# Optimization experiments

Hardware: AMD Instinct MI355X
Metric: run time of the kernel (lower is better)

Reference implementation:

```python
import jax, jax.numpy as jnp
import numpy as np

N_AUTHORS = 50000
N_PAPERS = 100000
N_NODES = N_AUTHORS + N_PAPERS
N_EDGES = 1200000
EMB_DIM = 64
NUM_LAYERS = 3


def setup_inputs() -> dict:
    key = jax.random.key(0)
    k1, k2, k3, k4, k5 = jax.random.split(key, 5)
    author_embedding = jax.random.normal(k1, (N_AUTHORS, EMB_DIM), dtype=jnp.float32)
    paper_embedding = jax.random.normal(k2, (N_PAPERS, EMB_DIM), dtype=jnp.float32)
    adj_rows = jax.random.randint(k3, (N_EDGES,), 0, N_NODES, dtype=jnp.int32)
    adj_cols = jax.random.randint(k4, (N_EDGES,), 0, N_NODES, dtype=jnp.int32)
    # symmetric-normalized adjacency values are small positive floats
    adj_vals = jax.random.uniform(k5, (N_EDGES,), dtype=jnp.float32) * 0.1
    return {
        "author_embedding": author_embedding,
        "paper_embedding": paper_embedding,
        "adj_rows": adj_rows,
        "adj_cols": adj_cols,
        "adj_vals": adj_vals,
    }


def _spmm(adj_rows, adj_cols, adj_vals, x):
    # sparse [N,N] @ dense [N,d] via gather + segment_sum
    msgs = adj_vals[:, None] * x[adj_cols]  # [E, d]
    return jax.ops.segment_sum(msgs, adj_rows, num_segments=N_NODES)


def reference(author_embedding, paper_embedding, adj_rows, adj_cols, adj_vals):
    ego = jnp.concatenate([author_embedding, paper_embedding], axis=0)  # [N, d]
    acc = ego
    x = ego
    for _ in range(NUM_LAYERS):
        x = _spmm(adj_rows, adj_cols, adj_vals, x)
        acc = acc + x
    out = acc / jnp.float32(NUM_LAYERS + 1)  # mean over layer outputs
    out_author = out[:N_AUTHORS]
    out_paper = out[N_AUTHORS:]
    return ego, out_author, out_paper
```

## Files before the change

### kernel.cpp

```cpp
#include <hip/hip_runtime.h>

#define N_AUTHORS 50000
#define N_PAPERS  100000
#define N_NODES   150000
#define N_EDGES   1200000
#define EMB       64

#define BSHIFT 10
#define K_B    ((N_NODES + 1023) >> 10)
#define CHUNK  4096
#define NBLK_A ((N_EDGES + CHUNK - 1) / CHUNK)
#define NSC    (K_B * NBLK_A)
#define NBS1   ((NSC + 1023) / 1024)

typedef float v2f __attribute__((ext_vector_type(2)));

__device__ __forceinline__ ushort f2bf(float f) {
    unsigned u = __float_as_uint(f);
    return (ushort)((u + 0x7fffu + ((u >> 16) & 1u)) >> 16);
}
#define bfLO(u) __uint_as_float((u) << 16)
#define bfHI(u) __uint_as_float((u) & 0xffff0000u)

__global__ void lgcn_hist_init(const int* __restrict__ rows,
                               unsigned* __restrict__ counts,
                               const float* __restrict__ a,
                               const float* __restrict__ p,
                               float* __restrict__ ego_out,
                               ushort* __restrict__ x0) {
    __shared__ unsigned h[K_B];
    int t = threadIdx.x;
    if (blockIdx.x < NBLK_A) {
        for (int i = t; i < K_B; i += blockDim.x) h[i] = 0;
        __syncthreads();
        int base = blockIdx.x * CHUNK;
        int end  = base + CHUNK; if (end > N_EDGES) end = N_EDGES;
        for (int e = base + t; e < end; e += blockDim.x)
            atomicAdd(&h[rows[e] >> BSHIFT], 1u);
        __syncthreads();
        for (int i = t; i < K_B; i += blockDim.x)
            counts[(size_t)i * NBLK_A + blockIdx.x] = h[i];
    } else {
        size_t i = (size_t)(blockIdx.x - NBLK_A) * blockDim.x + t;
        const size_t n4  = (size_t)N_NODES  * EMB / 4;
        const size_t au4 = (size_t)N_AUTHORS * EMB / 4;
        if (i >= n4) return;
        float4 v = (i < au4) ? ((const float4*)a)[i] : ((const float4*)p)[i - au4];
        ((float4*)ego_out)[i] = v;
        ushort4 b;
        b.x = f2bf(v.x); b.y = f2bf(v.y); b.z = f2bf(v.z); b.w = f2bf(v.w);
        ((ushort4*)x0)[i] = b;
    }
}

__global__ void lgcn_scan_l1(const unsigned* __restrict__ counts,
                             unsigned* __restrict__ scanned,
                             unsigned* __restrict__ btot) {
    __shared__ unsigned s[1024];
    int t = threadIdx.x;
    int i = blockIdx.x * 1024 + t;
    unsigned v = (i < NSC) ? counts[i] : 0u;
    s[t] = v;
    __syncthreads();
    for (int d = 1; d < 1024; d <<= 1) {
        unsigned u = (t >= d) ? s[t - d] : 0u;
        __syncthreads();
        s[t] += u;
        __syncthreads();
    }
    if (i < NSC) scanned[i] = s[t] - v;
    if (t == 1023) btot[blockIdx.x] = s[1023];
}

__global__ void lgcn_scan_l2(const unsigned* __restrict__ btot,
                             unsigned* __restrict__ btot_ex) {
    __shared__ unsigned s[64];
    int t = threadIdx.x;
    unsigned v = (t < NBS1) ? btot[t] : 0u;
    s[t] = v;
    __syncthreads();
    for (int d = 1; d < 64; d <<= 1) {
        unsigned u = (t >= d) ? s[t - d] : 0u;
        __syncthreads();
        s[t] += u;
        __syncthreads();
    }
    btot_ex[t] = s[t] - v;
}

__device__ __forceinline__ unsigned scan_at(const unsigned* scanned,
                                            const unsigned* btot_ex, unsigned idx) {
    return scanned[idx] + btot_ex[idx >> 10];
}

__global__ void lgcn_a1_bin(const int* __restrict__ rows,
                            const int* __restrict__ cols,
                            const float* __restrict__ vals,
                            const unsigned* __restrict__ scanned,
                            const unsigned* __restrict__ btot_ex,
                            float2* __restrict__ stage) {
    __shared__ unsigned cur[K_B];
    int t = threadIdx.x;
    for (int i = t; i < K_B; i += blockDim.x)
        cur[i] = scan_at(scanned, btot_ex, (unsigned)i * NBLK_A + blockIdx.x);
    __syncthreads();
    int base = blockIdx.x * CHUNK;
    int end  = base + CHUNK; if (end > N_EDGES) end = N_EDGES;
    for (int e = base + t; e < end; e += blockDim.x) {
        int r = rows[e];
        unsigned pos = atomicAdd(&cur[r >> BSHIFT], 1u);
        unsigned packed = ((unsigned)(r & 1023) << 18) | (unsigned)cols[e];
        stage[pos] = make_float2(__uint_as_float(packed), vals[e]);
    }
}

__global__ void lgcn_place(const unsigned* __restrict__ scanned,
                           const unsigned* __restrict__ btot_ex,
                           const float2* __restrict__ stage,
                           float2* __restrict__ se,
                           unsigned* __restrict__ row_start) {
    __shared__ unsigned cur[1 << BSHIFT];
    __shared__ unsigned tsum[256];
    int b  = blockIdx.x;
    int rb = b << BSHIFT;
    int nrows = N_NODES - rb; if (nrows > (1 << BSHIFT)) nrows = 1 << BSHIFT;
    int t = threadIdx.x;

    unsigned base  = scan_at(scanned, btot_ex, (unsigned)b * NBLK_A);
    unsigned span1 = (b + 1 < K_B)
                   ? scan_at(scanned, btot_ex, (unsigned)(b + 1) * NBLK_A)
                   : N_EDGES;

    for (int i = t; i < (1 << BSHIFT); i += 256) cur[i] = 0;
    __syncthreads();
    for (unsigned p = base + t; p < span1; p += 256)
        atomicAdd(&cur[__float_as_uint(stage[p].x) >> 18], 1u);
    __syncthreads();

    unsigned c[4], s = 0;
#pragma unroll
    for (int k = 0; k < 4; ++k) { c[k] = cur[t * 4 + k]; s += c[k]; }
    tsum[t] = s;
    __syncthreads();
    for (int d = 1; d < 256; d <<= 1) {
        unsigned u = (t >= d) ? tsum[t - d] : 0u;
        __syncthreads();
        tsum[t] += u;
        __syncthreads();
    }
    unsigned run = base + (tsum[t] - s);
    __syncthreads();
#pragma unroll
    for (int k = 0; k < 4; ++k) {
        int i = t * 4 + k;
        cur[i] = run;
        if (i < nrows) row_start[rb + i] = run;
        run += c[k];
    }
    if (b == K_B - 1 && t == 0) row_start[N_NODES] = N_EDGES;
    __syncthreads();

    for (unsigned p = base + t; p < span1; p += 256) {
        float2 v = stage[p];
        unsigned u = __float_as_uint(v.x);
        unsigned pos = atomicAdd(&cur[u >> 18], 1u);
        se[pos] = make_float2(__int_as_float((int)(u & 0x3FFFFu)), v.y);
    }
}

template <int MODE>
__global__ void lgcn_spmm(const unsigned* __restrict__ rs,
                          const float2* __restrict__ se,
                          const ushort* __restrict__ xb,
                          const unsigned char* __restrict__ x8,
                          ushort* __restrict__ y16,
                          unsigned char* __restrict__ y8,
                          const ushort* __restrict__ egob,
                          const ushort* __restrict__ y1b,
                          float* __restrict__ out) {
    int w    = blockIdx.x * (blockDim.x >> 6) + (threadIdx.x >> 6);
    int lane = threadIdx.x & 63;
    int r0   = w << 1;
    if (r0 >= N_NODES) return;
    unsigned jA   = rs[r0];
    unsigned endA = rs[r0 + 1];
    unsigned jB   = endA;
    unsigned endB = rs[r0 + 2];
    const int g  = lane >> 3;
    const int d8 = (lane & 7) << 3;
    float a0=0.f,a1=0.f,a2=0.f,a3=0.f,a4=0.f,a5=0.f,a6=0.f,a7=0.f;
    float b0=0.f,b1=0.f,b2=0.f,b3=0.f,b4=0.f,b5=0.f,b6=0.f,b7=0.f;

#define BATCH8(JB, END, P)                                                    \
    {                                                                         \
        unsigned idx = (JB) + g;                                              \
        float2 e;                                                             \
        if (idx < (END)) e = se[idx];                                         \
        else { e.x = __int_as_float(0); e.y = 0.f; }                          \
        if constexpr (MODE == 0) {                                            \
            const uint4 xv = *(const uint4*)(xb + ((size_t)__float_as_int(e.x) << 6) + d8); \
            P##0 += e.y * bfLO(xv.x); P##1 += e.y * bfHI(xv.x);               \
            P##2 += e.y * bfLO(xv.y); P##3 += e.y * bfHI(xv.y);               \
            P##4 += e.y * bfLO(xv.z); P##5 += e.y * bfHI(xv.z);               \
            P##6 += e.y * bfLO(xv.w); P##7 += e.y * bfHI(xv.w);               \
        } else {                                                              \
            const uint2 xv = *(const uint2*)(x8 + ((size_t)__float_as_int(e.x) << 6) + d8); \
            v2f p01 = __builtin_amdgcn_cvt_pk_f32_fp8((int)xv.x, false);      \
            v2f p23 = __builtin_amdgcn_cvt_pk_f32_fp8((int)xv.x, true);       \
            v2f p45 = __builtin_amdgcn_cvt_pk_f32_fp8((int)xv.y, false);      \
            v2f p67 = __builtin_amdgcn_cvt_pk_f32_fp8((int)xv.y, true);       \
            P##0 += e.y * p01.x; P##1 += e.y * p01.y;                         \
            P##2 += e.y * p23.x; P##3 += e.y * p23.y;                         \
            P##4 += e.y * p45.x; P##5 += e.y * p45.y;                         \
            P##6 += e.y * p67.x; P##7 += e.y * p67.y;                         \
        }                                                                     \
    }

    BATCH8(jA, endA, a)
    BATCH8(jB, endB, b)
    jA += 8; jB += 8;
    while (jA < endA) { BATCH8(jA, endA, a) jA += 8; }
    while (jB < endB) { BATCH8(jB, endB, b) jB += 8; }
#undef BATCH8

    a0 += __shfl_xor(a0, 8, 64); a0 += __shfl_xor(a0, 16, 64); a0 += __shfl_xor(a0, 32, 64);
    a1 += __shfl_xor(a1, 8, 64); a1 += __shfl_xor(a1, 16, 64); a1 += __shfl_xor(a1, 32, 64);
    a2 += __shfl_xor(a2, 8, 64); a2 += __shfl_xor(a2, 16, 64); a2 += __shfl_xor(a2, 32, 64);
    a3 += __shfl_xor(a3, 8, 64); a3 += __shfl_xor(a3, 16, 64); a3 += __shfl_xor(a3, 32, 64);
    a4 += __shfl_xor(a4, 8, 64); a4 += __shfl_xor(a4, 16, 64); a4 += __shfl_xor(a4, 32, 64);
    a5 += __shfl_xor(a5, 8, 64); a5 += __shfl_xor(a5, 16, 64); a5 += __shfl_xor(a5, 32, 64);
    a6 += __shfl_xor(a6, 8, 64); a6 += __shfl_xor(a6, 16, 64); a6 += __shfl_xor(a6, 32, 64);
    a7 += __shfl_xor(a7, 8, 64); a7 += __shfl_xor(a7, 16, 64); a7 += __shfl_xor(a7, 32, 64);
    b0 += __shfl_xor(b0, 8, 64); b0 += __shfl_xor(b0, 16, 64); b0 += __shfl_xor(b0, 32, 64);
    b1 += __shfl_xor(b1, 8, 64); b1 += __shfl_xor(b1, 16, 64); b1 += __shfl_xor(b1, 32, 64);
    b2 += __shfl_xor(b2, 8, 64); b2 += __shfl_xor(b2, 16, 64); b2 += __shfl_xor(b2, 32, 64);
    b3 += __shfl_xor(b3, 8, 64); b3 += __shfl_xor(b3, 16, 64); b3 += __shfl_xor(b3, 32, 64);
    b4 += __shfl_xor(b4, 8, 64); b4 += __shfl_xor(b4, 16, 64); b4 += __shfl_xor(b4, 32, 64);
    b5 += __shfl_xor(b5, 8, 64); b5 += __shfl_xor(b5, 16, 64); b5 += __shfl_xor(b5, 32, 64);
    b6 += __shfl_xor(b6, 8, 64); b6 += __shfl_xor(b6, 16, 64); b6 += __shfl_xor(b6, 32, 64);
    b7 += __shfl_xor(b7, 8, 64); b7 += __shfl_xor(b7, 16, 64); b7 += __shfl_xor(b7, 32, 64);

    if (g == 0) {
#define EMIT(ROW, P)                                                          \
    {                                                                         \
        size_t o = ((size_t)(ROW) << 6) + d8;                                 \
        if constexpr (MODE == 2) {                                            \
            uint4 ue = *(const uint4*)(egob + o);                             \
            uint4 u1 = *(const uint4*)(y1b + o);                              \
            uint2 u2 = *(const uint2*)(x8 + o);                               \
            v2f q01 = __builtin_amdgcn_cvt_pk_f32_fp8((int)u2.x, false);      \
            v2f q23 = __builtin_amdgcn_cvt_pk_f32_fp8((int)u2.x, true);       \
            v2f q45 = __builtin_amdgcn_cvt_pk_f32_fp8((int)u2.y, false);      \
            v2f q67 = __builtin_amdgcn_cvt_pk_f32_fp8((int)u2.y, true);       \
            float4 lo, hi;                                                    \
            lo.x = 0.25f * (bfLO(ue.x) + bfLO(u1.x) + q01.x + P##0);          \
            lo.y = 0.25f * (bfHI(ue.x) + bfHI(u1.x) + q01.y + P##1);          \
            lo.z = 0.25f * (bfLO(ue.y) + bfLO(u1.y) + q23.x + P##2);          \
            lo.w = 0.25f * (bfHI(ue.y) + bfHI(u1.y) + q23.y + P##3);          \
            hi.x = 0.25f * (bfLO(ue.z) + bfLO(u1.z) + q45.x + P##4);          \
            hi.y = 0.25f * (bfHI(ue.z) + bfHI(u1.z) + q45.y + P##5);          \
            hi.z = 0.25f * (bfLO(ue.w) + bfLO(u1.w) + q67.x + P##6);          \
            hi.w = 0.25f * (bfHI(ue.w) + bfHI(u1.w) + q67.y + P##7);          \
            *(float4*)(out + o)     = lo;                                     \
            *(float4*)(out + o + 4) = hi;                                     \
        } else {                                                              \
            int w0 = __builtin_amdgcn_cvt_pk_fp8_f32(P##0, P##1, 0, false);   \
            w0     = __builtin_amdgcn_cvt_pk_fp8_f32(P##2, P##3, w0, true);   \
            int w1 = __builtin_amdgcn_cvt_pk_fp8_f32(P##4, P##5, 0, false);   \
            w1     = __builtin_amdgcn_cvt_pk_fp8_f32(P##6, P##7, w1, true);   \
            uint2 ov8; ov8.x = (unsigned)w0; ov8.y = (unsigned)w1;            \
            *(uint2*)(y8 + o) = ov8;                                          \
            if constexpr (MODE == 0) {                                        \
                uint4 ov;                                                     \
                ov.x = (unsigned)f2bf(P##0) | ((unsigned)f2bf(P##1) << 16);   \
                ov.y = (unsigned)f2bf(P##2) | ((unsigned)f2bf(P##3) << 16);   \
                ov.z = (unsigned)f2bf(P##4) | ((unsigned)f2bf(P##5) << 16);   \
                ov.w = (unsigned)f2bf(P##6) | ((unsigned)f2bf(P##7) << 16);   \
                *(uint4*)(y16 + o) = ov;                                      \
            }                                                                 \
        }                                                                     \
    }
        EMIT(r0, a)
        EMIT(r0 + 1, b)
#undef EMIT
    }
}

extern "C" void kernel_launch(void* const* d_in, const int* in_sizes, int n_in,
                              void* d_out, int out_size, void* d_ws, size_t ws_size,
                              hipStream_t stream) {
    const float* author = (const float*)d_in[0];
    const float* paper  = (const float*)d_in[1];
    const int*   rows   = (const int*)d_in[2];
    const int*   cols   = (const int*)d_in[3];
    const float* vals   = (const float*)d_in[4];

    float* ego_out = (float*)d_out;
    float* acc     = (float*)d_out + (size_t)N_NODES * EMB;

    char* w = (char*)d_ws;
    float2*   se        = (float2*)w;   w += (size_t)N_EDGES * sizeof(float2);
    float2*   stage     = (float2*)w;   w += (size_t)N_EDGES * sizeof(float2);
    ushort*   xbE       = (ushort*)w;   w += (size_t)N_NODES * EMB * sizeof(ushort);
    ushort*   xb1       = (ushort*)w;   w += (size_t)N_NODES * EMB * sizeof(ushort);
    unsigned char* y2_8 = (unsigned char*)w; w += (size_t)N_NODES * EMB;
    unsigned* row_start = (unsigned*)w; w += (size_t)(N_NODES + 1) * 4;
    unsigned* bcounts   = (unsigned*)w; w += (size_t)NSC * 4;
    unsigned* bscanned  = (unsigned*)w; w += (size_t)NSC * 4;
    unsigned* btot      = (unsigned*)w; w += 64 * 4;
    unsigned* btot_ex   = (unsigned*)w; w += 64 * 4;
    unsigned char* y1_8 = (unsigned char*)stage;

    const int BLK = 256;
    const int g_vec  = (int)(((size_t)N_NODES * EMB / 4 + BLK - 1) / BLK);
    const int g_spmm = ((N_NODES / 2) + 3) / 4;

    lgcn_hist_init<<<NBLK_A + g_vec, BLK, 0, stream>>>(rows, bcounts,
                                                       author, paper, ego_out, xbE);

    lgcn_scan_l1<<<NBS1, 1024, 0, stream>>>(bcounts, bscanned, btot);
    lgcn_scan_l2<<<1, 64, 0, stream>>>(btot, btot_ex);

    lgcn_a1_bin<<<NBLK_A, BLK, 0, stream>>>(rows, cols, vals, bscanned, btot_ex, stage);
    lgcn_place<<<K_B, BLK, 0, stream>>>(bscanned, btot_ex, stage, se, row_start);

    lgcn_spmm<0><<<g_spmm, BLK, 0, stream>>>(row_start, se, xbE, nullptr,
                                             xb1, y1_8, nullptr, nullptr, nullptr);
    lgcn_spmm<1><<<g_spmm, BLK, 0, stream>>>(row_start, se, nullptr, y1_8,
                                             nullptr, y2_8, nullptr, nullptr, nullptr);
    lgcn_spmm<2><<<g_spmm, BLK, 0, stream>>>(row_start, se, nullptr, y2_8,
                                             nullptr, nullptr, xbE, xb1, acc);
}
```

Measured before the change: 193.5 us.

## Fold second-level scan into consumers, drop bf16 layer-1 copy, pack math into v2f

Removes the one-block scan_l2 kernel. Each a1_bin and place block instead computes the small block-total prefix serially in shared memory. It also stops writing a bf16 copy of layer 1 and has the final layer read the fp8 layer-1 buffer, which cuts global writes and reads. Accumulators are restructured into float2 vectors to enable packed FMA and shuffles. The costs are lower precision for the layer-1 term in the output and a small serial prefix per block.

```diff
diff --git a/kernel.cpp b/kernel.cpp
--- a/kernel.cpp
+++ b/kernel.cpp
@@ -21,6 +21,20 @@
 }
 #define bfLO(u) __uint_as_float((u) << 16)
 #define bfHI(u) __uint_as_float((u) & 0xffff0000u)
+
+__device__ __forceinline__ v2f mkv2(float a, float b) { v2f r; r.x = a; r.y = b; return r; }
+__device__ __forceinline__ v2f bfv2(unsigned u) { return mkv2(bfLO(u), bfHI(u)); }
+
+__device__ __forceinline__ v2f red_v2(v2f v) {
+#pragma unroll
+    for (int s = 8; s <= 32; s <<= 1) {
+        v2f o;
+        o.x = __shfl_xor(v.x, s, 64);
+        o.y = __shfl_xor(v.y, s, 64);
+        v += o;
+    }
+    return v;
+}
 
 __global__ void lgcn_hist_init(const int* __restrict__ rows,
                                unsigned* __restrict__ counts,
@@ -72,37 +86,29 @@
     if (t == 1023) btot[blockIdx.x] = s[1023];
 }
 
-__global__ void lgcn_scan_l2(const unsigned* __restrict__ btot,
-                             unsigned* __restrict__ btot_ex) {
-    __shared__ unsigned s[64];
-    int t = threadIdx.x;
-    unsigned v = (t < NBS1) ? btot[t] : 0u;
-    s[t] = v;
-    __syncthreads();
-    for (int d = 1; d < 64; d <<= 1) {
-        unsigned u = (t >= d) ? s[t - d] : 0u;
-        __syncthreads();
-        s[t] += u;
-        __syncthreads();
-    }
-    btot_ex[t] = s[t] - v;
-}
-
-__device__ __forceinline__ unsigned scan_at(const unsigned* scanned,
-                                            const unsigned* btot_ex, unsigned idx) {
-    return scanned[idx] + btot_ex[idx >> 10];
+__device__ __forceinline__ void btot_prefix(const unsigned* __restrict__ btot,
+                                            unsigned* __restrict__ btex) {
+    if (threadIdx.x == 0) {
+        unsigned run = 0;
+        for (int i = 0; i < NBS1; ++i) { btex[i] = run; run += btot[i]; }
+    }
+    __syncthreads();
 }
 
 __global__ void lgcn_a1_bin(const int* __restrict__ rows,
                             const int* __restrict__ cols,
                             const float* __restrict__ vals,
                             const unsigned* __restrict__ scanned,
-                            const unsigned* __restrict__ btot_ex,
+                            const unsigned* __restrict__ btot,
                             float2* __restrict__ stage) {
     __shared__ unsigned cur[K_B];
+    __shared__ unsigned btex[NBS1];
+    btot_prefix(btot, btex);
     int t = threadIdx.x;
-    for (int i = t; i < K_B; i += blockDim.x)
-        cur[i] = scan_at(scanned, btot_ex, (unsigned)i * NBLK_A + blockIdx.x);
+    for (int i = t; i < K_B; i += blockDim.x) {
+        unsigned idx = (unsigned)i * NBLK_A + blockIdx.x;
+        cur[i] = scanned[idx] + btex[idx >> 10];
+    }
     __syncthreads();
     int base = blockIdx.x * CHUNK;
     int end  = base + CHUNK; if (end > N_EDGES) end = N_EDGES;
@@ -115,21 +121,26 @@
 }
 
 __global__ void lgcn_place(const unsigned* __restrict__ scanned,
-                           const unsigned* __restrict__ btot_ex,
+                           const unsigned* __restrict__ btot,
                            const float2* __restrict__ stage,
                            float2* __restrict__ se,
                            unsigned* __restrict__ row_start) {
     __shared__ unsigned cur[1 << BSHIFT];
     __shared__ unsigned tsum[256];
+    __shared__ unsigned btex[NBS1];
+    btot_prefix(btot, btex);
     int b  = blockIdx.x;
     int rb = b << BSHIFT;
     int nrows = N_NODES - rb; if (nrows > (1 << BSHIFT)) nrows = 1 << BSHIFT;
     int t = threadIdx.x;
 
-    unsigned base  = scan_at(scanned, btot_ex, (unsigned)b * NBLK_A);
-    unsigned span1 = (b + 1 < K_B)
-                   ? scan_at(scanned, btot_ex, (unsigned)(b + 1) * NBLK_A)
-                   : N_EDGES;
+    unsigned i0 = (unsigned)b * NBLK_A;
+    unsigned base = scanned[i0] + btex[i0 >> 10];
+    unsigned span1;
+    if (b + 1 < K_B) {
+        unsigned i1 = (unsigned)(b + 1) * NBLK_A;
+        span1 = scanned[i1] + btex[i1 >> 10];
+    } else span1 = N_EDGES;
 
     for (int i = t; i < (1 << BSHIFT); i += 256) cur[i] = 0;
     __syncthreads();
@@ -173,10 +184,9 @@
                           const float2* __restrict__ se,
                           const ushort* __restrict__ xb,
                           const unsigned char* __restrict__ x8,
-                          ushort* __restrict__ y16,
                           unsigned char* __restrict__ y8,
                           const ushort* __restrict__ egob,
-                          const ushort* __restrict__ y1b,
+                          const unsigned char* __restrict__ y18,
                           float* __restrict__ out) {
     int w    = blockIdx.x * (blockDim.x >> 6) + (threadIdx.x >> 6);
     int lane = threadIdx.x & 63;
@@ -188,100 +198,74 @@
     unsigned endB = rs[r0 + 2];
     const int g  = lane >> 3;
     const int d8 = (lane & 7) << 3;
-    float a0=0.f,a1=0.f,a2=0.f,a3=0.f,a4=0.f,a5=0.f,a6=0.f,a7=0.f;
-    float b0=0.f,b1=0.f,b2=0.f,b3=0.f,b4=0.f,b5=0.f,b6=0.f,b7=0.f;
-
-#define BATCH8(JB, END, P)                                                    \
+    v2f A0 = {0.f, 0.f}, A1 = A0, A2 = A0, A3 = A0;
+    v2f B0 = A0, B1 = A0, B2 = A0, B3 = A0;
+
+#define BATCH8(JB, END, P0, P1, P2, P3)                                       \
     {                                                                         \
         unsigned idx = (JB) + g;                                              \
         float2 e;                                                             \
         if (idx < (END)) e = se[idx];                                         \
         else { e.x = __int_as_float(0); e.y = 0.f; }                          \
+        v2f ey = mkv2(e.y, e.y);                                              \
         if constexpr (MODE == 0) {                                            \
             const uint4 xv = *(const uint4*)(xb + ((size_t)__float_as_int(e.x) << 6) + d8); \
-            P##0 += e.y * bfLO(xv.x); P##1 += e.y * bfHI(xv.x);               \
-            P##2 += e.y * bfLO(xv.y); P##3 += e.y * bfHI(xv.y);               \
-            P##4 += e.y * bfLO(xv.z); P##5 += e.y * bfHI(xv.z);               \
-            P##6 += e.y * bfLO(xv.w); P##7 += e.y * bfHI(xv.w);               \
+            P0 += ey * bfv2(xv.x);                                            \
+            P1 += ey * bfv2(xv.y);                                            \
+            P2 += ey * bfv2(xv.z);                                            \
+            P3 += ey * bfv2(xv.w);                                            \
         } else {                                                              \
             const uint2 xv = *(const uint2*)(x8 + ((size_t)__float_as_int(e.x) << 6) + d8); \
-            v2f p01 = __builtin_amdgcn_cvt_pk_f32_fp8((int)xv.x, false);      \
-            v2f p23 = __builtin_amdgcn_cvt_pk_f32_fp8((int)xv.x, true);       \
-            v2f p45 = __builtin_amdgcn_cvt_pk_f32_fp8((int)xv.y, false);      \
-            v2f p67 = __builtin_amdgcn_cvt_pk_f32_fp8((int)xv.y, true);       \
-            P##0 += e.y * p01.x; P##1 += e.y * p01.y;                         \
-            P##2 += e.y * p23.x; P##3 += e.y * p23.y;                         \
-            P##4 += e.y * p45.x; P##5 += e.y * p45.y;                         \
-            P##6 += e.y * p67.x; P##7 += e.y * p67.y;                         \
+            P0 += ey * __builtin_amdgcn_cvt_pk_f32_fp8((int)xv.x, false);     \
+            P1 += ey * __builtin_amdgcn_cvt_pk_f32_fp8((int)xv.x, true);      \
+            P2 += ey * __builtin_amdgcn_cvt_pk_f32_fp8((int)xv.y, false);     \
+            P3 += ey * __builtin_amdgcn_cvt_pk_f32_fp8((int)xv.y, true);      \
         }                                                                     \
     }
 
-    BATCH8(jA, endA, a)
-    BATCH8(jB, endB, b)
+    BATCH8(jA, endA, A0, A1, A2, A3)
+    BATCH8(jB, endB, B0, B1, B2, B3)
     jA += 8; jB += 8;
-    while (jA < endA) { BATCH8(jA, endA, a) jA += 8; }
-    while (jB < endB) { BATCH8(jB, endB, b) jB += 8; }
+    while (jA < endA) { BATCH8(jA, endA, A0, A1, A2, A3) jA += 8; }
+    while (jB < endB) { BATCH8(jB, endB, B0, B1, B2, B3) jB += 8; }
 #undef BATCH8
 
-    a0 += __shfl_xor(a0, 8, 64); a0 += __shfl_xor(a0, 16, 64); a0 += __shfl_xor(a0, 32, 64);
-    a1 += __shfl_xor(a1, 8, 64); a1 += __shfl_xor(a1, 16, 64); a1 += __shfl_xor(a1, 32, 64);
-    a2 += __shfl_xor(a2, 8, 64); a2 += __shfl_xor(a2, 16, 64); a2 += __shfl_xor(a2, 32, 64);
-    a3 += __shfl_xor(a3, 8, 64); a3 += __shfl_xor(a3, 16, 64); a3 += __shfl_xor(a3, 32, 64);
-    a4 += __shfl_xor(a4, 8, 64); a4 += __shfl_xor(a4, 16, 64); a4 += __shfl_xor(a4, 32, 64);
-    a5 += __shfl_xor(a5, 8, 64); a5 += __shfl_xor(a5, 16, 64); a5 += __shfl_xor(a5, 32, 64);
-    a6 += __shfl_xor(a6, 8, 64); a6 += __shfl_xor(a6, 16, 64); a6 += __shfl_xor(a6, 32, 64);
-    a7 += __shfl_xor(a7, 8, 64); a7 += __shfl_xor(a7, 16, 64); a7 += __shfl_xor(a7, 32, 64);
-    b0 += __shfl_xor(b0, 8, 64); b0 += __shfl_xor(b0, 16, 64); b0 += __shfl_xor(b0, 32, 64);
-    b1 += __shfl_xor(b1, 8, 64); b1 += __shfl_xor(b1, 16, 64); b1 += __shfl_xor(b1, 32, 64);
-    b2 += __shfl_xor(b2, 8, 64); b2 += __shfl_xor(b2, 16, 64); b2 += __shfl_xor(b2, 32, 64);
-    b3 += __shfl_xor(b3, 8, 64); b3 += __shfl_xor(b3, 16, 64); b3 += __shfl_xor(b3, 32, 64);
-    b4 += __shfl_xor(b4, 8, 64); b4 += __shfl_xor(b4, 16, 64); b4 += __shfl_xor(b4, 32, 64);
-    b5 += __shfl_xor(b5, 8, 64); b5 += __shfl_xor(b5, 16, 64); b5 += __shfl_xor(b5, 32, 64);
-    b6 += __shfl_xor(b6, 8, 64); b6 += __shfl_xor(b6, 16, 64); b6 += __shfl_xor(b6, 32, 64);
-    b7 += __shfl_xor(b7, 8, 64); b7 += __shfl_xor(b7, 16, 64); b7 += __shfl_xor(b7, 32, 64);
+    A0 = red_v2(A0); A1 = red_v2(A1); A2 = red_v2(A2); A3 = red_v2(A3);
+    B0 = red_v2(B0); B1 = red_v2(B1); B2 = red_v2(B2); B3 = red_v2(B3);
 
     if (g == 0) {
-#define EMIT(ROW, P)                                                          \
+#define EMIT(ROW, P0, P1, P2, P3)                                             \
     {                                                                         \
         size_t o = ((size_t)(ROW) << 6) + d8;                                 \
         if constexpr (MODE == 2) {                                            \
             uint4 ue = *(const uint4*)(egob + o);                             \
-            uint4 u1 = *(const uint4*)(y1b + o);                              \
+            uint2 u1 = *(const uint2*)(y18 + o);                              \
             uint2 u2 = *(const uint2*)(x8 + o);                               \
-            v2f q01 = __builtin_amdgcn_cvt_pk_f32_fp8((int)u2.x, false);      \
-            v2f q23 = __builtin_amdgcn_cvt_pk_f32_fp8((int)u2.x, true);       \
-            v2f q45 = __builtin_amdgcn_cvt_pk_f32_fp8((int)u2.y, false);      \
-            v2f q67 = __builtin_amdgcn_cvt_pk_f32_fp8((int)u2.y, true);       \
+            v2f q = mkv2(0.25f, 0.25f);                                       \
+            v2f r0 = (bfv2(ue.x) + __builtin_amdgcn_cvt_pk_f32_fp8((int)u1.x, false) \
+                      + __builtin_amdgcn_cvt_pk_f32_fp8((int)u2.x, false) + P0) * q; \
+            v2f r1 = (bfv2(ue.y) + __builtin_amdgcn_cvt_pk_f32_fp8((int)u1.x, true)  \
+                      + __builtin_amdgcn_cvt_pk_f32_fp8((int)u2.x, true) + P1) * q; \
+            v2f r2 = (bfv2(ue.z) + __builtin_amdgcn_cvt_pk_f32_fp8((int)u1.y, false) \
+                      + __builtin_amdgcn_cvt_pk_f32_fp8((int)u2.y, false) + P2) * q; \
+            v2f r3 = (bfv2(ue.w) + __builtin_amdgcn_cvt_pk_f32_fp8((int)u1.y, true)  \
+                      + __builtin_amdgcn_cvt_pk_f32_fp8((int)u2.y, true) + P3) * q; \
             float4 lo, hi;                                                    \
-            lo.x = 0.25f * (bfLO(ue.x) + bfLO(u1.x) + q01.x + P##0);          \
-            lo.y = 0.25f * (bfHI(ue.x) + bfHI(u1.x) + q01.y + P##1);          \
-            lo.z = 0.25f * (bfLO(ue.y) + bfLO(u1.y) + q23.x + P##2);          \
-            lo.w = 0.25f * (bfHI(ue.y) + bfHI(u1.y) + q23.y + P##3);          \
-            hi.x = 0.25f * (bfLO(ue.z) + bfLO(u1.z) + q45.x + P##4);          \
-            hi.y = 0.25f * (bfHI(ue.z) + bfHI(u1.z) + q45.y + P##5);          \
-            hi.z = 0.25f * (bfLO(ue.w) + bfLO(u1.w) + q67.x + P##6);          \
-            hi.w = 0.25f * (bfHI(ue.w) + bfHI(u1.w) + q67.y + P##7);          \
+            lo.x = r0.x; lo.y = r0.y; lo.z = r1.x; lo.w = r1.y;               \
+            hi.x = r2.x; hi.y = r2.y; hi.z = r3.x; hi.w = r3.y;               \
             *(float4*)(out + o)     = lo;                                     \
             *(float4*)(out + o + 4) = hi;                                     \
         } else {                                                              \
-            int w0 = __builtin_amdgcn_cvt_pk_fp8_f32(P##0, P##1, 0, false);   \
-            w0     = __builtin_amdgcn_cvt_pk_fp8_f32(P##2, P##3, w0, true);   \
-            int w1 = __builtin_amdgcn_cvt_pk_fp8_f32(P##4, P##5, 0, false);   \
-            w1     = __builtin_amdgcn_cvt_pk_fp8_f32(P##6, P##7, w1, true);   \
+            int w0 = __builtin_amdgcn_cvt_pk_fp8_f32(P0.x, P0.y, 0, false);   \
+            w0     = __builtin_amdgcn_cvt_pk_fp8_f32(P1.x, P1.y, w0, true);   \
+            int w1 = __builtin_amdgcn_cvt_pk_fp8_f32(P2.x, P2.y, 0, false);   \
+            w1     = __builtin_amdgcn_cvt_pk_fp8_f32(P3.x, P3.y, w1, true);   \
             uint2 ov8; ov8.x = (unsigned)w0; ov8.y = (unsigned)w1;            \
             *(uint2*)(y8 + o) = ov8;                                          \
-            if constexpr (MODE == 0) {                                        \
-                uint4 ov;                                                     \
-                ov.x = (unsigned)f2bf(P##0) | ((unsigned)f2bf(P##1) << 16);   \
-                ov.y = (unsigned)f2bf(P##2) | ((unsigned)f2bf(P##3) << 16);   \
-                ov.z = (unsigned)f2bf(P##4) | ((unsigned)f2bf(P##5) << 16);   \
-                ov.w = (unsigned)f2bf(P##6) | ((unsigned)f2bf(P##7) << 16);   \
-                *(uint4*)(y16 + o) = ov;                                      \
-            }                                                                 \
         }                                                                     \
     }
-        EMIT(r0, a)
-        EMIT(r0 + 1, b)
+        EMIT(r0, A0, A1, A2, A3)
+        EMIT(r0 + 1, B0, B1, B2, B3)
 #undef EMIT
     }
 }
@@ -302,13 +286,11 @@
     float2*   se        = (float2*)w;   w += (size_t)N_EDGES * sizeof(float2);
     float2*   stage     = (float2*)w;   w += (size_t)N_EDGES * sizeof(float2);
     ushort*   xbE       = (ushort*)w;   w += (size_t)N_NODES * EMB * sizeof(ushort);
-    ushort*   xb1       = (ushort*)w;   w += (size_t)N_NODES * EMB * sizeof(ushort);
     unsigned char* y2_8 = (unsigned char*)w; w += (size_t)N_NODES * EMB;
     unsigned* row_start = (unsigned*)w; w += (size_t)(N_NODES + 1) * 4;
     unsigned* bcounts   = (unsigned*)w; w += (size_t)NSC * 4;
     unsigned* bscanned  = (unsigned*)w; w += (size_t)NSC * 4;
     unsigned* btot      = (unsigned*)w; w += 64 * 4;
-    unsigned* btot_ex   = (unsigned*)w; w += 64 * 4;
     unsigned char* y1_8 = (unsigned char*)stage;
 
     const int BLK = 256;
@@ -319,15 +301,14 @@
                                                        author, paper, ego_out, xbE);
 
     lgcn_scan_l1<<<NBS1, 1024, 0, stream>>>(bcounts, bscanned, btot);
-    lgcn_scan_l2<<<1, 64, 0, stream>>>(btot, btot_ex);
-
-    lgcn_a1_bin<<<NBLK_A, BLK, 0, stream>>>(rows, cols, vals, bscanned, btot_ex, stage);
-    lgcn_place<<<K_B, BLK, 0, stream>>>(bscanned, btot_ex, stage, se, row_start);
+
+    lgcn_a1_bin<<<NBLK_A, BLK, 0, stream>>>(rows, cols, vals, bscanned, btot, stage);
+    lgcn_place<<<K_B, BLK, 0, stream>>>(bscanned, btot, stage, se, row_start);
 
     lgcn_spmm<0><<<g_spmm, BLK, 0, stream>>>(row_start, se, xbE, nullptr,
-                                             xb1, y1_8, nullptr, nullptr, nullptr);
+                                             y1_8, nullptr, nullptr, nullptr);
     lgcn_spmm<1><<<g_spmm, BLK, 0, stream>>>(row_start, se, nullptr, y1_8,
-                                             nullptr, y2_8, nullptr, nullptr, nullptr);
+                                             y2_8, nullptr, nullptr, nullptr);
     lgcn_spmm<2><<<g_spmm, BLK, 0, stream>>>(row_start, se, nullptr, y2_8,
-                                             nullptr, nullptr, xbE, xb1, acc);
-}
+                                             nullptr, xbE, y1_8, acc);
+}
```

Result: no change. 191.9 us (median of 2 runs) (-0.8%).
